# Optimization experiments

Hardware: AMD Instinct MI355X
Metric: run time of the kernel (lower is better)

The kernel has to match this reference:

```python
import jax, jax.numpy as jnp
import numpy as np

GRID_SIZE = 5
SPLINE_ORDER = 3
KK = 3  # kernel side
N_CONVS = 4
GRID_LO, GRID_HI = -1.0, 1.0


def b_splines(x, grid, k):
    # x: (N, in_features), grid: (grid_size + 2k + 1,) shared across in_features
    # returns (N, in_features, grid_size + k)
    x = x[..., None]
    bases = ((x >= grid[:-1]) & (x < grid[1:])).astype(x.dtype)
    for p in range(1, k + 1):
        left = (x - grid[:-(p + 1)]) / (grid[p:-1] - grid[:-(p + 1)])
        right = (grid[p + 1:] - x) / (grid[p + 1:] - grid[1:-p])
        bases = left * bases[..., :-1] + right * bases[..., 1:]
    return bases


def setup_inputs() -> dict:
    key = jax.random.key(0)
    k1, k2, k3, k4 = jax.random.split(key, 4)
    in_f = KK * KK
    x = jax.random.normal(k1, (8, 16, 96, 96), dtype=jnp.float32)
    # per-conv KANLinear params (out_features = 1), stacked over n_convs
    base_w = jax.random.normal(k2, (N_CONVS, in_f), dtype=jnp.float32) * (1.0 / np.sqrt(in_f))
    spline_w = jax.random.normal(k3, (N_CONVS, in_f, GRID_SIZE + SPLINE_ORDER), dtype=jnp.float32) * 0.1
    spline_scaler = jax.random.normal(k4, (N_CONVS, in_f), dtype=jnp.float32) * (1.0 / np.sqrt(in_f))
    h = (GRID_HI - GRID_LO) / GRID_SIZE
    grid = jnp.arange(-SPLINE_ORDER, GRID_SIZE + SPLINE_ORDER + 1, dtype=jnp.float32) * h + GRID_LO
    return {"x": x, "base_w": base_w, "spline_w": spline_w,
            "spline_scaler": spline_scaler, "grid": grid}


def reference(x, base_w, spline_w, spline_scaler, grid):
    B, C, H, W = x.shape
    # unfold (im2col): (B, C*KK*KK, Ho, Wo), feature dim ordered channel-slowest like torch Unfold
    patches = jax.lax.conv_general_dilated_patches(x, (KK, KK), (1, 1), 'VALID')
    Ho, Wo = patches.shape[2], patches.shape[3]
    # (B, C, Ho, Wo, KK*KK) -> flat rows (N, in_features)
    p = patches.reshape(B, C, KK * KK, Ho, Wo).transpose(0, 1, 3, 4, 2).reshape(-1, KK * KK)
    bases = b_splines(p, grid, SPLINE_ORDER)              # (N, in, G+k)
    sw = spline_w * spline_scaler[..., None]              # scaled spline weight (c, in, G+k)
    out = (jnp.einsum('ni,ci->nc', jax.nn.silu(p), base_w)
           + jnp.einsum('nig,cig->nc', bases, sw))        # (N, n_convs)
    # output channel index = kern + channel * n_convs
    out = out.reshape(B, C, Ho, Wo, N_CONVS).transpose(0, 1, 4, 2, 3)
    return out.reshape(B, C * N_CONVS, Ho, Wo)
```

## Files before the change

kernel.cpp:

```cpp
#include <hip/hip_runtime.h>
#include <math.h>

constexpr int Bb = 8, Cc = 16, Hh = 96, Ww = 96;
constexpr int Ho = 94, Wo = 94;
constexpr int NC = 4;
constexpr int PLANE = Ho * Wo;

constexpr int TX = 16;
constexpr int TYS = 47;
constexpr int IX = 18, IY = 49;
constexpr int NXT = 6, NYT = 2;
constexpr int FS = 12;
constexpr int ROWU = IX * FS;
constexpr int ROWB = ROWU * 2;

typedef __attribute__((ext_vector_type(4))) float f32x4;
typedef __attribute__((ext_vector_type(8))) short bf16x8;

__device__ __forceinline__ unsigned short f2bf(float f) {
    union { float f; unsigned u; } a; a.f = f;
    unsigned r = a.u + 0x7fffu + ((a.u >> 16) & 1u);
    return (unsigned short)(r >> 16);
}
__device__ __forceinline__ unsigned pk2(float a, float b) {
    return (unsigned)f2bf(a) | ((unsigned)f2bf(b) << 16);
}
__device__ __forceinline__ bf16x8 mkfrag(unsigned a0, unsigned a1, unsigned a2, unsigned a3) {
    union { unsigned u[4]; bf16x8 v; } t;
    t.u[0] = a0; t.u[1] = a1; t.u[2] = a2; t.u[3] = a3;
    return t.v;
}
__device__ __forceinline__ int recIdx(int i, int r) {
    return ((i / 3) * IX + r + (i % 3)) * FS;
}

struct F4 { float v0, v1, v2, v3; } __attribute__((packed, aligned(4)));

#define LD2(p, off) (*reinterpret_cast<const uint2*>((const char*)(p) + (off)))

__global__ __launch_bounds__(256, 6)
void kan_conv_kernel(const float* __restrict__ x,
                     const float* __restrict__ base_w,
                     const float* __restrict__ spline_w,
                     const float* __restrict__ spline_scaler,
                     const float* __restrict__ grid,
                     float* __restrict__ out)
{
    __shared__ unsigned short feat[IY * ROWU];
    __shared__ unsigned short Bw[16 * 128];

    const int tid = threadIdx.x;
    int blk = blockIdx.x;
    const int xt = blk % NXT; blk /= NXT;
    const int yt = blk % NYT; blk /= NYT;
    const int c  = blk % Cc;
    const int b  = blk / Cc;
    const int ox0 = xt * TX;
    const int oy0 = yt * TYS;

    {
        const int cv = tid >> 4;
        const int k0 = (tid & 15) * 8;
        unsigned d0 = 0, d1 = 0, d2 = 0, d3 = 0;
        if (cv < NC) {
            float w0=0,w1=0,w2=0,w3=0,w4=0,w5=0,w6=0,w7=0;
#pragma unroll
            for (int e = 0; e < 8; ++e) {
                const int k = k0 + e;
                float val = 0.f;
                if (k < 108) {
                    const int i  = k / 12;
                    const int cc = k - 12 * i;
                    const int wi = cv * 9 + i;
                    if (cc < 8)       val = spline_scaler[wi] * spline_w[wi * 8 + cc];
                    else if (cc == 8) val = base_w[wi];
                }
                if      (e == 0) w0 = val; else if (e == 1) w1 = val;
                else if (e == 2) w2 = val; else if (e == 3) w3 = val;
                else if (e == 4) w4 = val; else if (e == 5) w5 = val;
                else if (e == 6) w6 = val; else              w7 = val;
            }
            d0 = pk2(w0, w1); d1 = pk2(w2, w3); d2 = pk2(w4, w5); d3 = pk2(w6, w7);
        }
        *reinterpret_cast<uint4*>(&Bw[cv * 128 + k0]) = make_uint4(d0, d1, d2, d3);
    }

    const float g0   = grid[0];
    const float invh = 1.0f / (grid[1] - g0);
    const float* xplane = x + (size_t)(b * Cc + c) * Hh * Ww;

    for (int p = tid; p < IX * IY; p += 256) {
        const int py = p / IX, px = p % IX;
        const int gy = oy0 + py;
        const int gx = ox0 + px;
        const float v = (gx < Ww) ? xplane[gy * Ww + gx] : 0.0f;

        const float sl = v / (1.0f + __expf(-v));

        const float u = (v - g0) * invh;
        int j = (int)u;
        if (!(u >= 0.0f && u < 11.0f)) j = -100;
        const float t  = u - (float)j;
        const float t2 = t * t, t3 = t2 * t;
        const float omt = 1.0f - t;
        const float B0 = (1.0f / 6.0f) * omt * omt * omt;
        const float B1 = (1.0f / 6.0f) * (3.0f * t3 - 6.0f * t2 + 4.0f);
        const float B2 = (1.0f / 6.0f) * (-3.0f * t3 + 3.0f * t2 + 3.0f * t + 1.0f);
        const float B3 = (1.0f / 6.0f) * t3;

        float bb[8];
#pragma unroll
        for (int k = 0; k < 8; ++k) {
            float r = 0.0f;
            r = (j == k + 3) ? B0 : r;
            r = (j == k + 2) ? B1 : r;
            r = (j == k + 1) ? B2 : r;
            r = (j == k    ) ? B3 : r;
            bb[k] = r;
        }

        unsigned short* fp = &feat[p * FS];
        *reinterpret_cast<uint2*>(fp + 0) = make_uint2(pk2(bb[0], bb[1]), pk2(bb[2], bb[3]));
        *reinterpret_cast<uint2*>(fp + 4) = make_uint2(pk2(bb[4], bb[5]), pk2(bb[6], bb[7]));
        *reinterpret_cast<uint2*>(fp + 8) = make_uint2(pk2(sl, 0.0f), 0u);
    }

    __syncthreads();

    const int lane = tid & 63;
    const int wv   = tid >> 6;
    const int r    = lane & 15;
    const int g    = lane >> 4;

    const bf16x8 bb0 = *reinterpret_cast<const bf16x8*>(&Bw[r * 128 +  0 + g * 8]);
    const bf16x8 bb1 = *reinterpret_cast<const bf16x8*>(&Bw[r * 128 + 32 + g * 8]);
    const bf16x8 bb2 = *reinterpret_cast<const bf16x8*>(&Bw[r * 128 + 64 + g * 8]);
    const bf16x8 bb3 = *reinterpret_cast<const bf16x8*>(&Bw[r * 128 + 96 + g * 8]);

    const int kb0 = 8 * g, kb1 = 32 + 8 * g, kb2 = 64 + 8 * g;
    const int i0 = kb0 / 12, i1 = kb1 / 12, i2 = kb2 / 12;
    const int q0 = kb0 - 12 * i0, q1 = kb1 - 12 * i1, q2 = kb2 - 12 * i2;
    const char* fbp = (const char*)feat + wv * ROWB;
    const char* pA0 = fbp + 2 * (recIdx(i0, r) + q0);
    const char* pA1 = fbp + 2 * (recIdx(i1, r) + q1);
    const char* pAX = fbp + 2 * recIdx(i1 + 1, r);
    const char* pA2 = fbp + 2 * (recIdx(i2, r) + q2);
    const char* pA3 = fbp + 2 * ((2 * IX + r + 2) * FS);

    float* obase = out + ((size_t)((b * Cc + c) * NC) + r) * PLANE;

#pragma unroll
    for (int k = 0; k < 12; ++k) {
        const int oyl = wv + 4 * k;
        if (oyl >= TYS) continue;
        const int yb = k * (4 * ROWB);
        f32x4 acc = {0.f, 0.f, 0.f, 0.f};

        {
            const uint2 lo = LD2(pA0, yb), hi = LD2(pA0, yb + 8);
            acc = __builtin_amdgcn_mfma_f32_16x16x32_bf16(mkfrag(lo.x, lo.y, hi.x, hi.y), bb0, acc, 0, 0, 0);
        }
        {
            const uint2 lo = LD2(pA1, yb), hi = LD2(pA1, yb + 8);
            const uint2 xlo = LD2(pAX, yb);
            const unsigned h0 = (g == 0) ? xlo.x : hi.x;
            const unsigned h1 = (g == 0) ? xlo.y : hi.y;
            acc = __builtin_amdgcn_mfma_f32_16x16x32_bf16(mkfrag(lo.x, lo.y, h0, h1), bb1, acc, 0, 0, 0);
        }
        {
            const uint2 lo = LD2(pA2, yb), hi = LD2(pA2, yb + 8);
            acc = __builtin_amdgcn_mfma_f32_16x16x32_bf16(mkfrag(lo.x, lo.y, hi.x, hi.y), bb2, acc, 0, 0, 0);
        }
        {
            const uint2 q01 = LD2(pA3, yb), q23 = LD2(pA3, yb + 8), q45 = LD2(pA3, yb + 16);
            const unsigned l0 = (g == 0) ? q01.x : ((g == 1) ? q45.x : 0u);
            const unsigned l1 = (g == 0) ? q01.y : 0u;
            const unsigned h0 = (g == 0) ? q23.x : 0u;
            const unsigned h1 = (g == 0) ? q23.y : 0u;
            acc = __builtin_amdgcn_mfma_f32_16x16x32_bf16(mkfrag(l0, l1, h0, h1), bb3, acc, 0, 0, 0);
        }

        if (r < NC) {
            const int oy = oy0 + oyl;
            const int oxs = ox0 + g * 4;
            float* op = obase + oy * Wo + oxs;
            if (oxs + 3 < Wo) {
                F4 s; s.v0 = acc[0]; s.v1 = acc[1]; s.v2 = acc[2]; s.v3 = acc[3];
                *reinterpret_cast<F4*>(op) = s;
            } else {
#pragma unroll
                for (int e = 0; e < 4; ++e)
                    if (oxs + e < Wo) op[e] = acc[e];
            }
        }
    }
}

extern "C" void kernel_launch(void* const* d_in, const int* in_sizes, int n_in,
                              void* d_out, int out_size, void* d_ws, size_t ws_size,
                              hipStream_t stream) {
    const float* x             = (const float*)d_in[0];
    const float* base_w        = (const float*)d_in[1];
    const float* spline_w      = (const float*)d_in[2];
    const float* spline_scaler = (const float*)d_in[3];
    const float* grid          = (const float*)d_in[4];
    float* out = (float*)d_out;

    const int nblocks = Bb * Cc * NXT * NYT;
    kan_conv_kernel<<<nblocks, 256, 0, stream>>>(x, base_w, spline_w,
                                                 spline_scaler, grid, out);
}
```

Measured before the change: 21.66 us.

## Reuse input rows across output rows via per-row partial MFMAs and DPP shifts

Each wave now processes a contiguous band of 12 output rows. It computes the per-input-row contribution once for all three kernel rows, packing 12 output columns (3 kernel-row slots times 4 convs) into the MFMA N dimension. Partial results from the three preceding input rows are combined with DPP row shifts before the store. This cuts the MFMA count per output row from four to about two, and removes the irregular A-fragment gathers. In exchange the kernel computes two extra input rows per wave, adds cross-lane DPP adds, and pads shared memory.

```diff
diff --git a/kernel.cpp b/kernel.cpp
--- a/kernel.cpp
+++ b/kernel.cpp
@@ -6,16 +6,18 @@
 constexpr int NC = 4;
 constexpr int PLANE = Ho * Wo;
 
-constexpr int TX = 16;
-constexpr int TYS = 47;
+constexpr int TX = 16, TYS = 47;
 constexpr int IX = 18, IY = 49;
 constexpr int NXT = 6, NYT = 2;
 constexpr int FS = 12;
 constexpr int ROWU = IX * FS;
 constexpr int ROWB = ROWU * 2;
+constexpr int BWS = 72;
 
 typedef __attribute__((ext_vector_type(4))) float f32x4;
 typedef __attribute__((ext_vector_type(8))) short bf16x8;
+
+template <int N> struct IC { static constexpr int value = N; };
 
 __device__ __forceinline__ unsigned short f2bf(float f) {
     union { float f; unsigned u; } a; a.f = f;
@@ -30,13 +32,14 @@
     t.u[0] = a0; t.u[1] = a1; t.u[2] = a2; t.u[3] = a3;
     return t.v;
 }
-__device__ __forceinline__ int recIdx(int i, int r) {
-    return ((i / 3) * IX + r + (i % 3)) * FS;
+__device__ __forceinline__ float dpp_shr4(float v) {
+    return __int_as_float(__builtin_amdgcn_update_dpp(0, __float_as_int(v), 0x114, 0xF, 0xF, true));
+}
+__device__ __forceinline__ float dpp_shr8(float v) {
+    return __int_as_float(__builtin_amdgcn_update_dpp(0, __float_as_int(v), 0x118, 0xF, 0xF, true));
 }
 
 struct F4 { float v0, v1, v2, v3; } __attribute__((packed, aligned(4)));
-
-#define LD2(p, off) (*reinterpret_cast<const uint2*>((const char*)(p) + (off)))
 
 __global__ __launch_bounds__(256, 6)
 void kan_conv_kernel(const float* __restrict__ x,
@@ -46,8 +49,8 @@
                      const float* __restrict__ grid,
                      float* __restrict__ out)
 {
-    __shared__ unsigned short feat[IY * ROWU];
-    __shared__ unsigned short Bw[16 * 128];
+    __shared__ unsigned short feat[IY * ROWU + 256];
+    __shared__ unsigned short Bw[16 * BWS];
 
     const int tid = threadIdx.x;
     int blk = blockIdx.x;
@@ -59,30 +62,26 @@
     const int oy0 = yt * TYS;
 
     {
-        const int cv = tid >> 4;
-        const int k0 = (tid & 15) * 8;
-        unsigned d0 = 0, d1 = 0, d2 = 0, d3 = 0;
-        if (cv < NC) {
-            float w0=0,w1=0,w2=0,w3=0,w4=0,w5=0,w6=0,w7=0;
+        const int col = tid >> 4;
+        const int k0  = (tid & 15) * 4;
+        const int d = col >> 2, cv = col & 3;
+        unsigned short w[4];
 #pragma unroll
-            for (int e = 0; e < 8; ++e) {
-                const int k = k0 + e;
-                float val = 0.f;
-                if (k < 108) {
-                    const int i  = k / 12;
-                    const int cc = k - 12 * i;
-                    const int wi = cv * 9 + i;
-                    if (cc < 8)       val = spline_scaler[wi] * spline_w[wi * 8 + cc];
-                    else if (cc == 8) val = base_w[wi];
-                }
-                if      (e == 0) w0 = val; else if (e == 1) w1 = val;
-                else if (e == 2) w2 = val; else if (e == 3) w3 = val;
-                else if (e == 4) w4 = val; else if (e == 5) w5 = val;
-                else if (e == 6) w6 = val; else              w7 = val;
+        for (int e = 0; e < 4; ++e) {
+            const int k = k0 + e;
+            float val = 0.f;
+            if (col < 12 && k < 36) {
+                const int j = k / 12, o = k - 12 * j;
+                const int wi = cv * 9 + 3 * d + j;
+                if (o < 8)       val = spline_scaler[wi] * spline_w[wi * 8 + o];
+                else if (o == 8) val = base_w[wi];
             }
-            d0 = pk2(w0, w1); d1 = pk2(w2, w3); d2 = pk2(w4, w5); d3 = pk2(w6, w7);
+            w[e] = f2bf(val);
         }
-        *reinterpret_cast<uint4*>(&Bw[cv * 128 + k0]) = make_uint4(d0, d1, d2, d3);
+        *reinterpret_cast<uint2*>(&Bw[col * BWS + k0]) =
+            make_uint2((unsigned)w[0] | ((unsigned)w[1] << 16),
+                       (unsigned)w[2] | ((unsigned)w[3] << 16));
+        feat[IY * ROWU + tid] = 0;
     }
 
     const float g0   = grid[0];
@@ -132,68 +131,66 @@
     const int r    = lane & 15;
     const int g    = lane >> 4;
 
-    const bf16x8 bb0 = *reinterpret_cast<const bf16x8*>(&Bw[r * 128 +  0 + g * 8]);
-    const bf16x8 bb1 = *reinterpret_cast<const bf16x8*>(&Bw[r * 128 + 32 + g * 8]);
-    const bf16x8 bb2 = *reinterpret_cast<const bf16x8*>(&Bw[r * 128 + 64 + g * 8]);
-    const bf16x8 bb3 = *reinterpret_cast<const bf16x8*>(&Bw[r * 128 + 96 + g * 8]);
-
-    const int kb0 = 8 * g, kb1 = 32 + 8 * g, kb2 = 64 + 8 * g;
-    const int i0 = kb0 / 12, i1 = kb1 / 12, i2 = kb2 / 12;
-    const int q0 = kb0 - 12 * i0, q1 = kb1 - 12 * i1, q2 = kb2 - 12 * i2;
-    const char* fbp = (const char*)feat + wv * ROWB;
-    const char* pA0 = fbp + 2 * (recIdx(i0, r) + q0);
-    const char* pA1 = fbp + 2 * (recIdx(i1, r) + q1);
-    const char* pAX = fbp + 2 * recIdx(i1 + 1, r);
-    const char* pA2 = fbp + 2 * (recIdx(i2, r) + q2);
-    const char* pA3 = fbp + 2 * ((2 * IX + r + 2) * FS);
-
-    float* obase = out + ((size_t)((b * Cc + c) * NC) + r) * PLANE;
-
+    const bf16x8 wb1 = *reinterpret_cast<const bf16x8*>(&Bw[r * BWS +  0 + 8 * g]);
+    const bf16x8 wb2 = *reinterpret_cast<const bf16x8*>(&Bw[r * BWS + 32 + 8 * g]);
+
+    const char* fb = (const char*)feat + (12 * wv) * ROWB + 24 * r + 16 * g;
+
+    const int cvl = r & 3;
+    float* obase = out + ((size_t)((b * Cc + c) * NC) + cvl) * PLANE;
+    const bool storer = (r >= 8) && (r < 12);
+    const int oxs = ox0 + 4 * g;
+    const bool fullstore = (oxs + 3 < Wo);
+
+    f32x4 sA, sB, sC;
+    const f32x4 zz = {0.f, 0.f, 0.f, 0.f};
+    sA = zz; sB = zz; sC = zz;
+
+    auto kstep = [&](auto ITC, f32x4& cur, f32x4& p1, f32x4& p2) {
+        constexpr int IT = decltype(ITC)::value;
+        const uint2 lo = *reinterpret_cast<const uint2*>(fb + IT * ROWB);
+        const uint2 hi = *reinterpret_cast<const uint2*>(fb + IT * ROWB + 8);
+        const uint2 x2 = *reinterpret_cast<const uint2*>(fb + IT * ROWB + 64);
+        cur = __builtin_amdgcn_mfma_f32_16x16x32_bf16(mkfrag(lo.x, lo.y, hi.x, hi.y), wb1, zz, 0, 0, 0);
+        cur = __builtin_amdgcn_mfma_f32_16x16x32_bf16(mkfrag(x2.x, x2.y, x2.x, x2.y), wb2, cur, 0, 0, 0);
+        if constexpr (IT >= 2) {
+            const int lrow = 12 * wv + IT - 2;
+            if (lrow < TYS) {
+                f32x4 tot;
+                tot[0] = cur[0] + dpp_shr4(p1[0]) + dpp_shr8(p2[0]);
+                tot[1] = cur[1] + dpp_shr4(p1[1]) + dpp_shr8(p2[1]);
+                tot[2] = cur[2] + dpp_shr4(p1[2]) + dpp_shr8(p2[2]);
+                tot[3] = cur[3] + dpp_shr4(p1[3]) + dpp_shr8(p2[3]);
+                if (storer) {
+                    const int oy = oy0 + lrow;
+                    float* op = obase + oy * Wo + oxs;
+                    if (fullstore) {
+                        F4 s; s.v0 = tot[0]; s.v1 = tot[1]; s.v2 = tot[2]; s.v3 = tot[3];
+                        *reinterpret_cast<F4*>(op) = s;
+                    } else {
 #pragma unroll
-    for (int k = 0; k < 12; ++k) {
-        const int oyl = wv + 4 * k;
-        if (oyl >= TYS) continue;
-        const int yb = k * (4 * ROWB);
-        f32x4 acc = {0.f, 0.f, 0.f, 0.f};
-
-        {
-            const uint2 lo = LD2(pA0, yb), hi = LD2(pA0, yb + 8);
-            acc = __builtin_amdgcn_mfma_f32_16x16x32_bf16(mkfrag(lo.x, lo.y, hi.x, hi.y), bb0, acc, 0, 0, 0);
-        }
-        {
-            const uint2 lo = LD2(pA1, yb), hi = LD2(pA1, yb + 8);
-            const uint2 xlo = LD2(pAX, yb);
-            const unsigned h0 = (g == 0) ? xlo.x : hi.x;
-            const unsigned h1 = (g == 0) ? xlo.y : hi.y;
-            acc = __builtin_amdgcn_mfma_f32_16x16x32_bf16(mkfrag(lo.x, lo.y, h0, h1), bb1, acc, 0, 0, 0);
-        }
-        {
-            const uint2 lo = LD2(pA2, yb), hi = LD2(pA2, yb + 8);
-            acc = __builtin_amdgcn_mfma_f32_16x16x32_bf16(mkfrag(lo.x, lo.y, hi.x, hi.y), bb2, acc, 0, 0, 0);
-        }
-        {
-            const uint2 q01 = LD2(pA3, yb), q23 = LD2(pA3, yb + 8), q45 = LD2(pA3, yb + 16);
-            const unsigned l0 = (g == 0) ? q01.x : ((g == 1) ? q45.x : 0u);
-            const unsigned l1 = (g == 0) ? q01.y : 0u;
-            const unsigned h0 = (g == 0) ? q23.x : 0u;
-            const unsigned h1 = (g == 0) ? q23.y : 0u;
-            acc = __builtin_amdgcn_mfma_f32_16x16x32_bf16(mkfrag(l0, l1, h0, h1), bb3, acc, 0, 0, 0);
-        }
-
-        if (r < NC) {
-            const int oy = oy0 + oyl;
-            const int oxs = ox0 + g * 4;
-            float* op = obase + oy * Wo + oxs;
-            if (oxs + 3 < Wo) {
-                F4 s; s.v0 = acc[0]; s.v1 = acc[1]; s.v2 = acc[2]; s.v3 = acc[3];
-                *reinterpret_cast<F4*>(op) = s;
-            } else {
-#pragma unroll
-                for (int e = 0; e < 4; ++e)
-                    if (oxs + e < Wo) op[e] = acc[e];
+                        for (int e = 0; e < 4; ++e)
+                            if (oxs + e < Wo) op[e] = tot[e];
+                    }
+                }
             }
         }
-    }
+    };
+
+    kstep(IC<0>{},  sA, sC, sB);
+    kstep(IC<1>{},  sB, sA, sC);
+    kstep(IC<2>{},  sC, sB, sA);
+    kstep(IC<3>{},  sA, sC, sB);
+    kstep(IC<4>{},  sB, sA, sC);
+    kstep(IC<5>{},  sC, sB, sA);
+    kstep(IC<6>{},  sA, sC, sB);
+    kstep(IC<7>{},  sB, sA, sC);
+    kstep(IC<8>{},  sC, sB, sA);
+    kstep(IC<9>{},  sA, sC, sB);
+    kstep(IC<10>{}, sB, sA, sC);
+    kstep(IC<11>{}, sC, sB, sA);
+    kstep(IC<12>{}, sA, sC, sB);
+    kstep(IC<13>{}, sB, sA, sC);
 }
 
 extern "C" void kernel_launch(void* const* d_in, const int* in_sizes, int n_in,
```

Result: faster. 20.04 us (-7.5%).
